# Optimization experiments

Hardware: AMD Instinct MI355X
Metric: run time of the kernel (lower is better)

Reference implementation:

```python
import jax, jax.numpy as jnp
import numpy as np

N_HEAD = 8
EPS = 1e-6  # LayerNorm2d eps


def setup_inputs() -> dict:
    key = jax.random.key(0)
    ks = jax.random.split(key, 7)
    B, C, H, W = 16, 256, 128, 128
    nh, dk, dv = N_HEAD, 32, 32
    s = 1.0 / np.sqrt(C)
    return {
        "q": jax.random.normal(ks[0], (B, C, H, W), jnp.float32),
        "k": jax.random.normal(ks[1], (B, C, H, W), jnp.float32),
        "v": jax.random.normal(ks[2], (B, C, H, W), jnp.float32),
        # 1x1 convs without bias == channel matmuls; weight shape [out_ch, in_ch]
        "wq": jax.random.normal(ks[3], (nh * dk, C), jnp.float32) * s,
        "wk": jax.random.normal(ks[4], (nh * dk, C), jnp.float32) * s,
        "wv": jax.random.normal(ks[5], (nh * dv, C), jnp.float32) * s,
        "wfc": jax.random.normal(ks[6], (C, nh * dv), jnp.float32) * (1.0 / np.sqrt(nh * dv)),
        "ln_w": jnp.ones((C,), jnp.float32),
        "ln_b": jnp.zeros((C,), jnp.float32),
        "kernel": 5,
        "pad": 2,
    }


def _forward(q, k, v, wq, wk, wv, wfc, ln_w, ln_b, kernel, pad):
    B, C, H, W = q.shape
    nh = N_HEAD
    dk = wq.shape[0] // nh
    dv = wv.shape[0] // nh
    assert kernel == 2 * pad + 1
    residual = q
    # 1x1 conv projections, split into heads: [B, nh, d, H, W]
    qh = jnp.einsum('oc,bchw->bohw', wq, q).reshape(B, nh, dk, H, W)
    kh = jnp.einsum('oc,bchw->bohw', wk, k).reshape(B, nh, dk, H, W)
    vh = jnp.einsum('oc,bchw->bohw', wv, v).reshape(B, nh, dv, H, W)
    # zero-pad spatially: out-of-bounds correlations/values are zero, matching the
    # original bilinear sampler (zeros padding) and the custom padding() helper.
    kp = jnp.pad(kh, ((0, 0), (0, 0), (0, 0), (pad, pad), (pad, pad)))
    vp = jnp.pad(vh, ((0, 0), (0, 0), (0, 0), (pad, pad), (pad, pad)))
    # local correlation volume: dot(q[i,j], k[i+dy-pad, j+dx-pad]) for the KxK window
    # (integer offsets -> bilinear sample degenerates to a gather). Never materializes
    # the full [B, HW, HW] matrix the torch code builds before sampling.
    corr = jnp.stack(
        [jnp.einsum('bncij,bncij->bnij', qh, kp[:, :, :, dy:dy + H, dx:dx + W])
         for dy in range(kernel) for dx in range(kernel)], axis=-1)  # [B,nh,H,W,K*K]
    # relu (from CorrBlock.corr), temperature = sqrt(d_k), softmax over window.
    # OOB entries are 0 (not -inf), faithfully matching the original.
    attn = jax.nn.softmax(jax.nn.relu(corr) / jnp.float32(np.sqrt(dk)), axis=-1)
    # channel attention: per-pixel weighted sum of v over the same window
    out = jnp.zeros((B, nh, dv, H, W), q.dtype)
    idx = 0
    for dy in range(kernel):
        for dx in range(kernel):
            out = out + attn[:, :, :, :, idx][:, :, None] * vp[:, :, :, dy:dy + H, dx:dx + W]
            idx += 1
    o = jnp.einsum('oc,bchw->bohw', wfc, out.reshape(B, nh * dv, H, W)) + residual
    # LayerNorm2d: normalize over channel dim per pixel
    mu = o.mean(1, keepdims=True)
    var = ((o - mu) ** 2).mean(1, keepdims=True)
    y = (o - mu) / jnp.sqrt(var + EPS)
    return ln_w[None, :, None, None] * y + ln_b[None, :, None, None]


def reference(q, k, v, wq, wk, wv, wfc, ln_w, ln_b, kernel, pad):
    return _forward(q, k, v, wq, wk, wv, wfc, ln_w, ln_b, kernel, pad)
```

## Files before the change

kernel.cpp:

```cpp
#include <hip/hip_runtime.h>
#include <hip/hip_bf16.h>

#define BATCH 16
#define CH 256
#define HH 128
#define WW 128
#define HWSZ (HH * WW)
#define NHEAD 8
#define DHEAD 32
#define LDST 40
#define PW 132
#define PPIX (132 * 132)

typedef __attribute__((ext_vector_type(8))) short bf16x8;
typedef __attribute__((ext_vector_type(4))) float f32x4;
typedef _Float16 h2v __attribute__((ext_vector_type(2)));

__device__ __forceinline__ unsigned short f2b(float f) {
    unsigned u = __builtin_bit_cast(unsigned, f);
    u += 0x7fffu + ((u >> 16) & 1u);
    return (unsigned short)(u >> 16);
}
__device__ __forceinline__ unsigned short f2h(float f) {
    _Float16 h = (_Float16)f;
    return __builtin_bit_cast(unsigned short, h);
}

#if __has_builtin(__builtin_amdgcn_fdot2)
#define DOT2(a, b, c) __builtin_amdgcn_fdot2((a), (b), (c), false)
#else
#define DOT2(a, b, c) ((c) + (float)(a).x * (float)(b).x + (float)(a).y * (float)(b).y)
#endif

__global__ __launch_bounds__(256)
void zpad_kernel(unsigned short* __restrict__ kpad, unsigned short* __restrict__ vpad)
{
    int bid = blockIdx.x;
    unsigned short* dst = ((bid & 1) ? vpad : kpad) + (size_t)(bid >> 1) * PPIX * DHEAD;
    const uint4 z = {0u, 0u, 0u, 0u};
    for (int i = threadIdx.x; i < 1040; i += 256) {
        int row, col;
        if (i < 264)      { row = i / 132; col = i - row * 132; }
        else if (i < 528) { int j = i - 264; int r = j / 132; row = 130 + r; col = j - r * 132; }
        else              { int j = i - 528; row = 2 + (j >> 2); int c = j & 3; col = (c < 2) ? c : (128 + c); }
        uint4* p = reinterpret_cast<uint4*>(dst + (size_t)(row * PW + col) * DHEAD);
        p[0] = z; p[1] = z; p[2] = z; p[3] = z;
    }
}

__global__ __launch_bounds__(256)
void prep_kernel(const float* __restrict__ wq, const float* __restrict__ wk,
                 const float* __restrict__ wv, unsigned short* __restrict__ wb)
{
    const float* src = (blockIdx.y == 0) ? wq : (blockIdx.y == 1) ? wk : wv;
    unsigned short* dst = wb + blockIdx.y * 65536;
    int e = (blockIdx.x * 256 + threadIdx.x) * 8;
    const float4* s = reinterpret_cast<const float4*>(src + e);
    float4 a = s[0], c = s[1];
    uint4 u;
    u.x = (unsigned)f2b(a.x) | ((unsigned)f2b(a.y) << 16);
    u.y = (unsigned)f2b(a.z) | ((unsigned)f2b(a.w) << 16);
    u.z = (unsigned)f2b(c.x) | ((unsigned)f2b(c.y) << 16);
    u.w = (unsigned)f2b(c.z) | ((unsigned)f2b(c.w) << 16);
    *reinterpret_cast<uint4*>(dst + e) = u;
}

__global__ __launch_bounds__(256)
void proj_kernel(const float* __restrict__ q, const float* __restrict__ k,
                 const float* __restrict__ v, const unsigned short* __restrict__ wb,
                 unsigned short* __restrict__ qh, unsigned short* __restrict__ kpad,
                 unsigned short* __restrict__ vpad)
{
    __shared__ __align__(16) unsigned short lA[256 * LDST];
    __shared__ __align__(16) unsigned short lB[64 * LDST];

    const int t = threadIdx.x;
    const int b = blockIdx.y;
    const int p0 = blockIdx.x * 64;
    const int z = blockIdx.z;

    const float* X; unsigned short* Y;
    if (z == 0)      { X = q; Y = qh; }
    else if (z == 1) { X = k; Y = kpad; }
    else             { X = v; Y = vpad; }
    const unsigned short* Wb = wb + z * 65536;
    X += (size_t)b * CH * HWSZ;
    const size_t pixstride = (z == 0) ? (size_t)HWSZ : (size_t)PPIX;
    Y += (size_t)b * NHEAD * pixstride * DHEAD;

    const int lane = t & 63;
    const int wid  = t >> 6;
    const int lrow = lane & 15;
    const int lkg  = lane >> 4;
    const int pB = t & 63;
    const int cg = t >> 6;

    f32x4 acc[4][4];
    const f32x4 zero = {0.f, 0.f, 0.f, 0.f};
#pragma unroll
    for (int m = 0; m < 4; ++m)
#pragma unroll
        for (int n = 0; n < 4; ++n) acc[m][n] = zero;

    for (int ks = 0; ks < 8; ++ks) {
        const int k0 = ks * 32;
#pragma unroll
        for (int r = 0; r < 4; ++r) {
            int idx = t + 256 * r;
            int o = idx >> 2, kc = idx & 3;
            uint4 wv4 = *reinterpret_cast<const uint4*>(Wb + o * 256 + k0 + kc * 8);
            *reinterpret_cast<uint4*>(&lA[o * LDST + kc * 8]) = wv4;
        }
        {
            const float* xp = X + (size_t)(k0 + cg * 8) * HWSZ + p0 + pB;
            float fv[8];
#pragma unroll
            for (int i = 0; i < 8; ++i) fv[i] = xp[(size_t)i * HWSZ];
            ushort4 h0, h1;
            h0.x = f2b(fv[0]); h0.y = f2b(fv[1]); h0.z = f2b(fv[2]); h0.w = f2b(fv[3]);
            h1.x = f2b(fv[4]); h1.y = f2b(fv[5]); h1.z = f2b(fv[6]); h1.w = f2b(fv[7]);
            *reinterpret_cast<ushort4*>(&lB[pB * LDST + cg * 8])     = h0;
            *reinterpret_cast<ushort4*>(&lB[pB * LDST + cg * 8 + 4]) = h1;
        }
        __syncthreads();

        bf16x8 af[4], bfv[4];
#pragma unroll
        for (int m = 0; m < 4; ++m)
            af[m] = *reinterpret_cast<const bf16x8*>(&lA[(wid * 64 + m * 16 + lrow) * LDST + lkg * 8]);
#pragma unroll
        for (int n = 0; n < 4; ++n)
            bfv[n] = *reinterpret_cast<const bf16x8*>(&lB[(n * 16 + lrow) * LDST + lkg * 8]);
#pragma unroll
        for (int m = 0; m < 4; ++m)
#pragma unroll
            for (int n = 0; n < 4; ++n)
                acc[m][n] = __builtin_amdgcn_mfma_f32_16x16x32_bf16(af[m], bfv[n], acc[m][n], 0, 0, 0);
        __syncthreads();
    }

    const int lr = lane >> 4, lc = lane & 15;
#pragma unroll
    for (int m = 0; m < 4; ++m)
#pragma unroll
        for (int n = 0; n < 4; ++n) {
            int o = wid * 64 + m * 16 + lr * 4;
            int hh_ = o >> 5, d0 = o & 31;
            int p = p0 + n * 16 + lc;
            ushort4 pk;
            pk.x = f2h(acc[m][n][0]); pk.y = f2h(acc[m][n][1]);
            pk.z = f2h(acc[m][n][2]); pk.w = f2h(acc[m][n][3]);
            size_t pix;
            if (z == 0) pix = (size_t)hh_ * HWSZ + p;
            else { int row = p >> 7, col = p & 127; pix = (size_t)hh_ * PPIX + (size_t)(row + 2) * PW + (col + 2); }
            *reinterpret_cast<ushort4*>(&Y[pix * DHEAD + d0]) = pk;
        }
}

__global__ __launch_bounds__(1024)
void attn_kernel(unsigned short* __restrict__ qh,
                 const unsigned short* __restrict__ kpad,
                 const unsigned short* __restrict__ vpad)
{
    const int t = threadIdx.x;
    const int swz = (blockIdx.x & 7) * 1024 + (blockIdx.x >> 3);
    const int bh = swz >> 6;
    const int tile = swz & 63;
    const int x0 = (tile & 7) * 16, y0 = (tile >> 3) * 16;
    const int qc = t & 3;
    const int px = (t >> 2) & 15;
    const int py = t >> 6;
    const int gx = x0 + px, gy = y0 + py;

    unsigned short* qp = qh + ((size_t)bh * HWSZ + gy * WW + gx) * DHEAD + qc * 8;
    const unsigned short* kb = kpad + (size_t)bh * PPIX * DHEAD + qc * 8;
    const unsigned short* vb = vpad + (size_t)bh * PPIX * DHEAD + qc * 8;

    union { uint4 u; h2v h2[4]; } Q;
    Q.u = *reinterpret_cast<const uint4*>(qp);

    float ew[25];
#pragma unroll
    for (int wy = 0; wy < 5; ++wy) {
        const unsigned short* krow = kb + (size_t)((gy + wy) * PW + gx) * DHEAD;
#pragma unroll
        for (int wx = 0; wx < 5; ++wx) {
            union { uint4 u; h2v h2[4]; } K;
            K.u = *reinterpret_cast<const uint4*>(krow + wx * DHEAD);
            float s = 0.f;
#pragma unroll
            for (int j = 0; j < 4; ++j)
                s = DOT2(Q.h2[j], K.h2[j], s);
            s += __shfl_xor(s, 1);
            s += __shfl_xor(s, 2);
            ew[wy * 5 + wx] = __expf(fmaxf(s, 0.f) * 0.17677669529663687f);
        }
    }

    float sum = 0.f;
#pragma unroll
    for (int i = 0; i < 25; ++i) sum += ew[i];
    const float inv = 1.f / sum;

    union { uint4 u; h2v h2[4]; } A;
    const h2v hz = {(_Float16)0.f, (_Float16)0.f};
#pragma unroll
    for (int j = 0; j < 4; ++j) A.h2[j] = hz;

#pragma unroll
    for (int wy = 0; wy < 5; ++wy) {
        const unsigned short* vrow = vb + (size_t)((gy + wy) * PW + gx) * DHEAD;
#pragma unroll
        for (int wx = 0; wx < 5; ++wx) {
            _Float16 wh = (_Float16)(ew[wy * 5 + wx] * inv);
            h2v w2 = {wh, wh};
            union { uint4 u; h2v h2[4]; } V;
            V.u = *reinterpret_cast<const uint4*>(vrow + wx * DHEAD);
#pragma unroll
            for (int j = 0; j < 4; ++j)
                A.h2[j] += w2 * V.h2[j];
        }
    }

    *reinterpret_cast<uint4*>(qp) = A.u;
}

__global__ __launch_bounds__(256)
void fcln_kernel(const unsigned short* __restrict__ ob, const float* __restrict__ wfc,
                 const float* __restrict__ qres, const float* __restrict__ lnw,
                 const float* __restrict__ lnb, float* __restrict__ out)
{
    __shared__ __align__(16) unsigned short lA[256 * LDST];
    __shared__ __align__(16) unsigned short lB[64 * LDST];
    __shared__ float lsum[4][64];
    __shared__ float lssq[4][64];

    const int t = threadIdx.x;
    const int b = blockIdx.y;
    const int p0 = blockIdx.x * 64;

    const int lane = t & 63;
    const int wid  = t >> 6;
    const int lrow = lane & 15;
    const int lkg  = lane >> 4;
    const int pxs = t >> 2, qcs = t & 3;

    f32x4 acc[4][4];
    const f32x4 zero = {0.f, 0.f, 0.f, 0.f};
#pragma unroll
    for (int m = 0; m < 4; ++m)
#pragma unroll
        for (int n = 0; n < 4; ++n) acc[m][n] = zero;

    for (int ks = 0; ks < 8; ++ks) {
        const int k0 = ks * 32;
        {
            const float4* wr = reinterpret_cast<const float4*>(wfc + t * 256 + k0);
#pragma unroll
            for (int i = 0; i < 8; ++i) {
                float4 f = wr[i];
                ushort4 hh;
                hh.x = f2b(f.x); hh.y = f2b(f.y); hh.z = f2b(f.z); hh.w = f2b(f.w);
                *reinterpret_cast<ushort4*>(&lA[t * LDST + i * 4]) = hh;
            }
        }
        {
            const unsigned short* obb = ob + (size_t)(b * NHEAD + ks) * HWSZ * DHEAD;
            uint4 bv = *reinterpret_cast<const uint4*>(obb + (size_t)(p0 + pxs) * DHEAD + qcs * 8);
            uint4 o4;
            {
                h2v h;
                h = __builtin_bit_cast(h2v, bv.x); o4.x = (unsigned)f2b((float)h.x) | ((unsigned)f2b((float)h.y) << 16);
                h = __builtin_bit_cast(h2v, bv.y); o4.y = (unsigned)f2b((float)h.x) | ((unsigned)f2b((float)h.y) << 16);
                h = __builtin_bit_cast(h2v, bv.z); o4.z = (unsigned)f2b((float)h.x) | ((unsigned)f2b((float)h.y) << 16);
                h = __builtin_bit_cast(h2v, bv.w); o4.w = (unsigned)f2b((float)h.x) | ((unsigned)f2b((float)h.y) << 16);
            }
            *reinterpret_cast<uint4*>(&lB[pxs * LDST + qcs * 8]) = o4;
        }
        __syncthreads();

        bf16x8 af[4], bfv[4];
#pragma unroll
        for (int m = 0; m < 4; ++m)
            af[m] = *reinterpret_cast<const bf16x8*>(&lA[(wid * 64 + m * 16 + lrow) * LDST + lkg * 8]);
#pragma unroll
        for (int n = 0; n < 4; ++n)
            bfv[n] = *reinterpret_cast<const bf16x8*>(&lB[(n * 16 + lrow) * LDST + lkg * 8]);
#pragma unroll
        for (int m = 0; m < 4; ++m)
#pragma unroll
            for (int n = 0; n < 4; ++n)
                acc[m][n] = __builtin_amdgcn_mfma_f32_16x16x32_bf16(af[m], bfv[n], acc[m][n], 0, 0, 0);
        __syncthreads();
    }

    const int lr = lane >> 4, lc = lane & 15;
    const float* qb = qres + (size_t)b * CH * HWSZ;
#pragma unroll
    for (int m = 0; m < 4; ++m)
#pragma unroll
        for (int n = 0; n < 4; ++n)
#pragma unroll
            for (int j = 0; j < 4; ++j) {
                int o = wid * 64 + m * 16 + lr * 4 + j;
                int p = p0 + n * 16 + lc;
                acc[m][n][j] += qb[(size_t)o * HWSZ + p];
            }

    float s[4], s2[4];
#pragma unroll
    for (int n = 0; n < 4; ++n) {
        float a = 0.f, c2 = 0.f;
#pragma unroll
        for (int m = 0; m < 4; ++m)
#pragma unroll
            for (int j = 0; j < 4; ++j) {
                float x = acc[m][n][j];
                a += x; c2 += x * x;
            }
        a  += __shfl_xor(a, 16);  a  += __shfl_xor(a, 32);
        c2 += __shfl_xor(c2, 16); c2 += __shfl_xor(c2, 32);
        s[n] = a; s2[n] = c2;
    }
    if (lane < 16) {
#pragma unroll
        for (int n = 0; n < 4; ++n) {
            lsum[wid][n * 16 + lane] = s[n];
            lssq[wid][n * 16 + lane] = s2[n];
        }
    }
    __syncthreads();

    float mu[4], rs[4];
#pragma unroll
    for (int n = 0; n < 4; ++n) {
        int p = n * 16 + lc;
        float ts = lsum[0][p] + lsum[1][p] + lsum[2][p] + lsum[3][p];
        float tq = lssq[0][p] + lssq[1][p] + lssq[2][p] + lssq[3][p];
        float m_ = ts * (1.f / 256.f);
        float v_ = tq * (1.f / 256.f) - m_ * m_;
        mu[n] = m_;
        rs[n] = rsqrtf(v_ + 1e-6f);
    }

    float* op = out + (size_t)b * CH * HWSZ;
#pragma unroll
    for (int m = 0; m < 4; ++m)
#pragma unroll
        for (int j = 0; j < 4; ++j) {
            int o = wid * 64 + m * 16 + lr * 4 + j;
            float g = lnw[o], bb = lnb[o];
#pragma unroll
            for (int n = 0; n < 4; ++n) {
                int p = p0 + n * 16 + lc;
                op[(size_t)o * HWSZ + p] = (acc[m][n][j] - mu[n]) * rs[n] * g + bb;
            }
        }
}

extern "C" void kernel_launch(void* const* d_in, const int* in_sizes, int n_in,
                              void* d_out, int out_size, void* d_ws, size_t ws_size,
                              hipStream_t stream) {
    const float* q   = (const float*)d_in[0];
    const float* k   = (const float*)d_in[1];
    const float* v   = (const float*)d_in[2];
    const float* wq  = (const float*)d_in[3];
    const float* wk  = (const float*)d_in[4];
    const float* wv  = (const float*)d_in[5];
    const float* wfc = (const float*)d_in[6];
    const float* lnw = (const float*)d_in[7];
    const float* lnb = (const float*)d_in[8];

    const size_t qsz = (size_t)BATCH * NHEAD * HWSZ * DHEAD;
    const size_t psz = (size_t)BATCH * NHEAD * PPIX * DHEAD;
    if (ws_size < (qsz + 2 * psz) * sizeof(unsigned short)) return;

    unsigned short* qh = (unsigned short*)d_ws;
    unsigned short* kp = qh + qsz;
    unsigned short* vp = kp + psz;
    unsigned short* wb = (unsigned short*)d_out;

    zpad_kernel<<<256, 256, 0, stream>>>(kp, vp);
    prep_kernel<<<dim3(32, 3), 256, 0, stream>>>(wq, wk, wv, wb);
    proj_kernel<<<dim3(HWSZ / 64, BATCH, 3), 256, 0, stream>>>(q, k, v, wb, qh, kp, vp);
    attn_kernel<<<8192, 1024, 0, stream>>>(qh, kp, vp);
    fcln_kernel<<<dim3(HWSZ / 64, BATCH), 256, 0, stream>>>(qh, wfc, q, lnw, lnb, (float*)d_out);
}
```

Before: 806.2 us.

## Read weights straight from global memory, double-buffer swizzled LDS tiles in projection GEMMs

```diff
diff --git a/kernel.cpp b/kernel.cpp
--- a/kernel.cpp
+++ b/kernel.cpp
@@ -8,7 +8,6 @@
 #define HWSZ (HH * WW)
 #define NHEAD 8
 #define DHEAD 32
-#define LDST 40
 #define PW 132
 #define PPIX (132 * 132)
 
@@ -50,9 +49,11 @@
 
 __global__ __launch_bounds__(256)
 void prep_kernel(const float* __restrict__ wq, const float* __restrict__ wk,
-                 const float* __restrict__ wv, unsigned short* __restrict__ wb)
-{
-    const float* src = (blockIdx.y == 0) ? wq : (blockIdx.y == 1) ? wk : wv;
+                 const float* __restrict__ wv, const float* __restrict__ wfc,
+                 unsigned short* __restrict__ wb)
+{
+    const float* src = (blockIdx.y == 0) ? wq : (blockIdx.y == 1) ? wk
+                     : (blockIdx.y == 2) ? wv : wfc;
     unsigned short* dst = wb + blockIdx.y * 65536;
     int e = (blockIdx.x * 256 + threadIdx.x) * 8;
     const float4* s = reinterpret_cast<const float4*>(src + e);
@@ -65,18 +66,17 @@
     *reinterpret_cast<uint4*>(dst + e) = u;
 }
 
-__global__ __launch_bounds__(256)
+__global__ __launch_bounds__(512)
 void proj_kernel(const float* __restrict__ q, const float* __restrict__ k,
                  const float* __restrict__ v, const unsigned short* __restrict__ wb,
                  unsigned short* __restrict__ qh, unsigned short* __restrict__ kpad,
                  unsigned short* __restrict__ vpad)
 {
-    __shared__ __align__(16) unsigned short lA[256 * LDST];
-    __shared__ __align__(16) unsigned short lB[64 * LDST];
+    __shared__ __align__(16) unsigned short lB[2][128 * 32];
 
     const int t = threadIdx.x;
     const int b = blockIdx.y;
-    const int p0 = blockIdx.x * 64;
+    const int p0 = blockIdx.x * 128;
     const int z = blockIdx.z;
 
     const float* X; unsigned short* Y;
@@ -90,10 +90,12 @@
 
     const int lane = t & 63;
     const int wid  = t >> 6;
+    const int wm   = wid & 3;
+    const int wn   = wid >> 2;
     const int lrow = lane & 15;
     const int lkg  = lane >> 4;
-    const int pB = t & 63;
-    const int cg = t >> 6;
+    const int pB   = t & 127;
+    const int cg   = t >> 7;
 
     f32x4 acc[4][4];
     const f32x4 zero = {0.f, 0.f, 0.f, 0.f};
@@ -104,39 +106,32 @@
 
     for (int ks = 0; ks < 8; ++ks) {
         const int k0 = ks * 32;
-#pragma unroll
-        for (int r = 0; r < 4; ++r) {
-            int idx = t + 256 * r;
-            int o = idx >> 2, kc = idx & 3;
-            uint4 wv4 = *reinterpret_cast<const uint4*>(Wb + o * 256 + k0 + kc * 8);
-            *reinterpret_cast<uint4*>(&lA[o * LDST + kc * 8]) = wv4;
-        }
         {
             const float* xp = X + (size_t)(k0 + cg * 8) * HWSZ + p0 + pB;
             float fv[8];
 #pragma unroll
             for (int i = 0; i < 8; ++i) fv[i] = xp[(size_t)i * HWSZ];
-            ushort4 h0, h1;
-            h0.x = f2b(fv[0]); h0.y = f2b(fv[1]); h0.z = f2b(fv[2]); h0.w = f2b(fv[3]);
-            h1.x = f2b(fv[4]); h1.y = f2b(fv[5]); h1.z = f2b(fv[6]); h1.w = f2b(fv[7]);
-            *reinterpret_cast<ushort4*>(&lB[pB * LDST + cg * 8])     = h0;
-            *reinterpret_cast<ushort4*>(&lB[pB * LDST + cg * 8 + 4]) = h1;
+            uint4 u;
+            u.x = (unsigned)f2b(fv[0]) | ((unsigned)f2b(fv[1]) << 16);
+            u.y = (unsigned)f2b(fv[2]) | ((unsigned)f2b(fv[3]) << 16);
+            u.z = (unsigned)f2b(fv[4]) | ((unsigned)f2b(fv[5]) << 16);
+            u.w = (unsigned)f2b(fv[6]) | ((unsigned)f2b(fv[7]) << 16);
+            *reinterpret_cast<uint4*>(&lB[ks & 1][pB * 32 + ((cg ^ (pB & 3)) << 3)]) = u;
         }
         __syncthreads();
 
         bf16x8 af[4], bfv[4];
 #pragma unroll
         for (int m = 0; m < 4; ++m)
-            af[m] = *reinterpret_cast<const bf16x8*>(&lA[(wid * 64 + m * 16 + lrow) * LDST + lkg * 8]);
+            af[m] = *reinterpret_cast<const bf16x8*>(Wb + (wm * 64 + m * 16 + lrow) * 256 + k0 + lkg * 8);
 #pragma unroll
         for (int n = 0; n < 4; ++n)
-            bfv[n] = *reinterpret_cast<const bf16x8*>(&lB[(n * 16 + lrow) * LDST + lkg * 8]);
+            bfv[n] = *reinterpret_cast<const bf16x8*>(&lB[ks & 1][(wn * 64 + n * 16 + lrow) * 32 + ((lkg ^ (lrow & 3)) << 3)]);
 #pragma unroll
         for (int m = 0; m < 4; ++m)
 #pragma unroll
             for (int n = 0; n < 4; ++n)
                 acc[m][n] = __builtin_amdgcn_mfma_f32_16x16x32_bf16(af[m], bfv[n], acc[m][n], 0, 0, 0);
-        __syncthreads();
     }
 
     const int lr = lane >> 4, lc = lane & 15;
@@ -144,9 +139,9 @@
     for (int m = 0; m < 4; ++m)
 #pragma unroll
         for (int n = 0; n < 4; ++n) {
-            int o = wid * 64 + m * 16 + lr * 4;
+            int o = wm * 64 + m * 16 + lr * 4;
             int hh_ = o >> 5, d0 = o & 31;
-            int p = p0 + n * 16 + lc;
+            int p = p0 + wn * 64 + n * 16 + lc;
             ushort4 pk;
             pk.x = f2h(acc[m][n][0]); pk.y = f2h(acc[m][n][1]);
             pk.z = f2h(acc[m][n][2]); pk.w = f2h(acc[m][n][3]);
@@ -225,25 +220,27 @@
     *reinterpret_cast<uint4*>(qp) = A.u;
 }
 
-__global__ __launch_bounds__(256)
-void fcln_kernel(const unsigned short* __restrict__ ob, const float* __restrict__ wfc,
+__global__ __launch_bounds__(512)
+void fcln_kernel(const unsigned short* __restrict__ ob, const unsigned short* __restrict__ wfcb,
                  const float* __restrict__ qres, const float* __restrict__ lnw,
                  const float* __restrict__ lnb, float* __restrict__ out)
 {
-    __shared__ __align__(16) unsigned short lA[256 * LDST];
-    __shared__ __align__(16) unsigned short lB[64 * LDST];
-    __shared__ float lsum[4][64];
-    __shared__ float lssq[4][64];
+    __shared__ __align__(16) unsigned short lB[2][128 * 32];
+    __shared__ float lsum[8][128];
+    __shared__ float lssq[8][128];
 
     const int t = threadIdx.x;
     const int b = blockIdx.y;
-    const int p0 = blockIdx.x * 64;
+    const int p0 = blockIdx.x * 128;
 
     const int lane = t & 63;
     const int wid  = t >> 6;
+    const int wm   = wid & 3;
+    const int wn   = wid >> 2;
     const int lrow = lane & 15;
     const int lkg  = lane >> 4;
-    const int pxs = t >> 2, qcs = t & 3;
+    const int pxs  = t >> 2;
+    const int qcs  = t & 3;
 
     f32x4 acc[4][4];
     const f32x4 zero = {0.f, 0.f, 0.f, 0.f};
@@ -254,16 +251,6 @@
 
     for (int ks = 0; ks < 8; ++ks) {
         const int k0 = ks * 32;
-        {
-            const float4* wr = reinterpret_cast<const float4*>(wfc + t * 256 + k0);
-#pragma unroll
-            for (int i = 0; i < 8; ++i) {
-                float4 f = wr[i];
-                ushort4 hh;
-                hh.x = f2b(f.x); hh.y = f2b(f.y); hh.z = f2b(f.z); hh.w = f2b(f.w);
-                *reinterpret_cast<ushort4*>(&lA[t * LDST + i * 4]) = hh;
-            }
-        }
         {
             const unsigned short* obb = ob + (size_t)(b * NHEAD + ks) * HWSZ * DHEAD;
             uint4 bv = *reinterpret_cast<const uint4*>(obb + (size_t)(p0 + pxs) * DHEAD + qcs * 8);
@@ -275,23 +262,22 @@
                 h = __builtin_bit_cast(h2v, bv.z); o4.z = (unsigned)f2b((float)h.x) | ((unsigned)f2b((float)h.y) << 16);
                 h = __builtin_bit_cast(h2v, bv.w); o4.w = (unsigned)f2b((float)h.x) | ((unsigned)f2b((float)h.y) << 16);
             }
-            *reinterpret_cast<uint4*>(&lB[pxs * LDST + qcs * 8]) = o4;
+            *reinterpret_cast<uint4*>(&lB[ks & 1][pxs * 32 + ((qcs ^ (pxs & 3)) << 3)]) = o4;
         }
         __syncthreads();
 
         bf16x8 af[4], bfv[4];
 #pragma unroll
         for (int m = 0; m < 4; ++m)
-            af[m] = *reinterpret_cast<const bf16x8*>(&lA[(wid * 64 + m * 16 + lrow) * LDST + lkg * 8]);
+            af[m] = *reinterpret_cast<const bf16x8*>(wfcb + (wm * 64 + m * 16 + lrow) * 256 + k0 + lkg * 8);
 #pragma unroll
         for (int n = 0; n < 4; ++n)
-            bfv[n] = *reinterpret_cast<const bf16x8*>(&lB[(n * 16 + lrow) * LDST + lkg * 8]);
+            bfv[n] = *reinterpret_cast<const bf16x8*>(&lB[ks & 1][(wn * 64 + n * 16 + lrow) * 32 + ((lkg ^ (lrow & 3)) << 3)]);
 #pragma unroll
         for (int m = 0; m < 4; ++m)
 #pragma unroll
             for (int n = 0; n < 4; ++n)
                 acc[m][n] = __builtin_amdgcn_mfma_f32_16x16x32_bf16(af[m], bfv[n], acc[m][n], 0, 0, 0);
-        __syncthreads();
     }
 
     const int lr = lane >> 4, lc = lane & 15;
@@ -302,8 +288,8 @@
         for (int n = 0; n < 4; ++n)
 #pragma unroll
             for (int j = 0; j < 4; ++j) {
-                int o = wid * 64 + m * 16 + lr * 4 + j;
-                int p = p0 + n * 16 + lc;
+                int o = wm * 64 + m * 16 + lr * 4 + j;
+                int p = p0 + wn * 64 + n * 16 + lc;
                 acc[m][n][j] += qb[(size_t)o * HWSZ + p];
             }
 
@@ -322,11 +308,12 @@
         c2 += __shfl_xor(c2, 16); c2 += __shfl_xor(c2, 32);
         s[n] = a; s2[n] = c2;
     }
+    __syncthreads();
     if (lane < 16) {
 #pragma unroll
         for (int n = 0; n < 4; ++n) {
-            lsum[wid][n * 16 + lane] = s[n];
-            lssq[wid][n * 16 + lane] = s2[n];
+            lsum[wid][wn * 64 + n * 16 + lane] = s[n];
+            lssq[wid][wn * 64 + n * 16 + lane] = s2[n];
         }
     }
     __syncthreads();
@@ -334,9 +321,9 @@
     float mu[4], rs[4];
 #pragma unroll
     for (int n = 0; n < 4; ++n) {
-        int p = n * 16 + lc;
-        float ts = lsum[0][p] + lsum[1][p] + lsum[2][p] + lsum[3][p];
-        float tq = lssq[0][p] + lssq[1][p] + lssq[2][p] + lssq[3][p];
+        int p = wn * 64 + n * 16 + lc;
+        float ts = lsum[wn * 4 + 0][p] + lsum[wn * 4 + 1][p] + lsum[wn * 4 + 2][p] + lsum[wn * 4 + 3][p];
+        float tq = lssq[wn * 4 + 0][p] + lssq[wn * 4 + 1][p] + lssq[wn * 4 + 2][p] + lssq[wn * 4 + 3][p];
         float m_ = ts * (1.f / 256.f);
         float v_ = tq * (1.f / 256.f) - m_ * m_;
         mu[n] = m_;
@@ -348,11 +335,11 @@
     for (int m = 0; m < 4; ++m)
 #pragma unroll
         for (int j = 0; j < 4; ++j) {
-            int o = wid * 64 + m * 16 + lr * 4 + j;
+            int o = wm * 64 + m * 16 + lr * 4 + j;
             float g = lnw[o], bb = lnb[o];
 #pragma unroll
             for (int n = 0; n < 4; ++n) {
-                int p = p0 + n * 16 + lc;
+                int p = p0 + wn * 64 + n * 16 + lc;
                 op[(size_t)o * HWSZ + p] = (acc[m][n][j] - mu[n]) * rs[n] * g + bb;
             }
         }
@@ -373,16 +360,16 @@
 
     const size_t qsz = (size_t)BATCH * NHEAD * HWSZ * DHEAD;
     const size_t psz = (size_t)BATCH * NHEAD * PPIX * DHEAD;
-    if (ws_size < (qsz + 2 * psz) * sizeof(unsigned short)) return;
+    if (ws_size < (qsz + 2 * psz + 4 * 65536) * sizeof(unsigned short)) return;
 
     unsigned short* qh = (unsigned short*)d_ws;
     unsigned short* kp = qh + qsz;
     unsigned short* vp = kp + psz;
-    unsigned short* wb = (unsigned short*)d_out;
+    unsigned short* wb = vp + psz;
 
     zpad_kernel<<<256, 256, 0, stream>>>(kp, vp);
-    prep_kernel<<<dim3(32, 3), 256, 0, stream>>>(wq, wk, wv, wb);
-    proj_kernel<<<dim3(HWSZ / 64, BATCH, 3), 256, 0, stream>>>(q, k, v, wb, qh, kp, vp);
+    prep_kernel<<<dim3(32, 4), 256, 0, stream>>>(wq, wk, wv, wfc, wb);
+    proj_kernel<<<dim3(HWSZ / 128, BATCH, 3), 512, 0, stream>>>(q, k, v, wb, qh, kp, vp);
     attn_kernel<<<8192, 1024, 0, stream>>>(qh, kp, vp);
-    fcln_kernel<<<dim3(HWSZ / 64, BATCH), 256, 0, stream>>>(qh, wfc, q, lnw, lnb, (float*)d_out);
-}
+    fcln_kernel<<<dim3(HWSZ / 128, BATCH), 512, 0, stream>>>(qh, wb + 3 * 65536, q, lnw, lnb, (float*)d_out);
+}
```

New measurement: 868.6 us. 1.08x slower.

## Double-buffer GEMM operands, load weights from global into registers, prebake bf16 wfc

Applied to the files above, without the earlier changes.

```diff
diff --git a/kernel.cpp b/kernel.cpp
--- a/kernel.cpp
+++ b/kernel.cpp
@@ -8,9 +8,9 @@
 #define HWSZ (HH * WW)
 #define NHEAD 8
 #define DHEAD 32
-#define LDST 40
 #define PW 132
 #define PPIX (132 * 132)
+#define LDSTB 40
 
 typedef __attribute__((ext_vector_type(8))) short bf16x8;
 typedef __attribute__((ext_vector_type(4))) float f32x4;
@@ -25,11 +25,15 @@
     _Float16 h = (_Float16)f;
     return __builtin_bit_cast(unsigned short, h);
 }
+__device__ __forceinline__ unsigned pkbf(float a, float b) {
+    __hip_bfloat162_raw r = __hip_bfloat162_raw(__float22bfloat162_rn(make_float2(a, b)));
+    return (unsigned)r.x | ((unsigned)r.y << 16);
+}
 
 #if __has_builtin(__builtin_amdgcn_fdot2)
 #define DOT2(a, b, c) __builtin_amdgcn_fdot2((a), (b), (c), false)
 #else
-#define DOT2(a, b, c) ((c) + (float)(a).x * (float)(b).x + (float)(a).y * (float)(b).y)
+#define DOT2(a, b, c) ((c) + (float)(a)[0] * (float)(b)[0] + (float)(a)[1] * (float)(b)[1])
 #endif
 
 __global__ __launch_bounds__(256)
@@ -50,18 +54,18 @@
 
 __global__ __launch_bounds__(256)
 void prep_kernel(const float* __restrict__ wq, const float* __restrict__ wk,
-                 const float* __restrict__ wv, unsigned short* __restrict__ wb)
-{
-    const float* src = (blockIdx.y == 0) ? wq : (blockIdx.y == 1) ? wk : wv;
+                 const float* __restrict__ wv, const float* __restrict__ wfc,
+                 unsigned short* __restrict__ wb)
+{
+    const float* src = (blockIdx.y == 0) ? wq : (blockIdx.y == 1) ? wk
+                     : (blockIdx.y == 2) ? wv : wfc;
     unsigned short* dst = wb + blockIdx.y * 65536;
     int e = (blockIdx.x * 256 + threadIdx.x) * 8;
     const float4* s = reinterpret_cast<const float4*>(src + e);
     float4 a = s[0], c = s[1];
     uint4 u;
-    u.x = (unsigned)f2b(a.x) | ((unsigned)f2b(a.y) << 16);
-    u.y = (unsigned)f2b(a.z) | ((unsigned)f2b(a.w) << 16);
-    u.z = (unsigned)f2b(c.x) | ((unsigned)f2b(c.y) << 16);
-    u.w = (unsigned)f2b(c.z) | ((unsigned)f2b(c.w) << 16);
+    u.x = pkbf(a.x, a.y); u.y = pkbf(a.z, a.w);
+    u.z = pkbf(c.x, c.y); u.w = pkbf(c.z, c.w);
     *reinterpret_cast<uint4*>(dst + e) = u;
 }
 
@@ -71,8 +75,7 @@
                  unsigned short* __restrict__ qh, unsigned short* __restrict__ kpad,
                  unsigned short* __restrict__ vpad)
 {
-    __shared__ __align__(16) unsigned short lA[256 * LDST];
-    __shared__ __align__(16) unsigned short lB[64 * LDST];
+    __shared__ __align__(16) unsigned short lB[2][64 * LDSTB];
 
     const int t = threadIdx.x;
     const int b = blockIdx.y;
@@ -92,8 +95,19 @@
     const int wid  = t >> 6;
     const int lrow = lane & 15;
     const int lkg  = lane >> 4;
-    const int pB = t & 63;
-    const int cg = t >> 6;
+    const int pB   = t & 63;
+    const int cg   = t >> 6;
+
+    float fv[8];
+    {
+        const float* xp = X + (size_t)(cg * 8) * HWSZ + p0 + pB;
+#pragma unroll
+        for (int i = 0; i < 8; ++i) fv[i] = xp[(size_t)i * HWSZ];
+    }
+    bf16x8 afc[4], afn[4];
+#pragma unroll
+    for (int m = 0; m < 4; ++m)
+        afc[m] = *reinterpret_cast<const bf16x8*>(Wb + (wid * 64 + m * 16 + lrow) * 256 + lkg * 8);
 
     f32x4 acc[4][4];
     const f32x4 zero = {0.f, 0.f, 0.f, 0.f};
@@ -103,40 +117,34 @@
         for (int n = 0; n < 4; ++n) acc[m][n] = zero;
 
     for (int ks = 0; ks < 8; ++ks) {
-        const int k0 = ks * 32;
-#pragma unroll
-        for (int r = 0; r < 4; ++r) {
-            int idx = t + 256 * r;
-            int o = idx >> 2, kc = idx & 3;
-            uint4 wv4 = *reinterpret_cast<const uint4*>(Wb + o * 256 + k0 + kc * 8);
-            *reinterpret_cast<uint4*>(&lA[o * LDST + kc * 8]) = wv4;
-        }
         {
-            const float* xp = X + (size_t)(k0 + cg * 8) * HWSZ + p0 + pB;
-            float fv[8];
+            uint4 u;
+            u.x = pkbf(fv[0], fv[1]); u.y = pkbf(fv[2], fv[3]);
+            u.z = pkbf(fv[4], fv[5]); u.w = pkbf(fv[6], fv[7]);
+            *reinterpret_cast<uint4*>(&lB[ks & 1][pB * LDSTB + cg * 8]) = u;
+        }
+        if (ks < 7) {
+            const float* xp = X + (size_t)((ks + 1) * 32 + cg * 8) * HWSZ + p0 + pB;
 #pragma unroll
             for (int i = 0; i < 8; ++i) fv[i] = xp[(size_t)i * HWSZ];
-            ushort4 h0, h1;
-            h0.x = f2b(fv[0]); h0.y = f2b(fv[1]); h0.z = f2b(fv[2]); h0.w = f2b(fv[3]);
-            h1.x = f2b(fv[4]); h1.y = f2b(fv[5]); h1.z = f2b(fv[6]); h1.w = f2b(fv[7]);
-            *reinterpret_cast<ushort4*>(&lB[pB * LDST + cg * 8])     = h0;
-            *reinterpret_cast<ushort4*>(&lB[pB * LDST + cg * 8 + 4]) = h1;
         }
         __syncthreads();
-
-        bf16x8 af[4], bfv[4];
+        if (ks < 7) {
+#pragma unroll
+            for (int m = 0; m < 4; ++m)
+                afn[m] = *reinterpret_cast<const bf16x8*>(Wb + (wid * 64 + m * 16 + lrow) * 256 + (ks + 1) * 32 + lkg * 8);
+        }
+        bf16x8 bfv[4];
+#pragma unroll
+        for (int n = 0; n < 4; ++n)
+            bfv[n] = *reinterpret_cast<const bf16x8*>(&lB[ks & 1][(n * 16 + lrow) * LDSTB + lkg * 8]);
 #pragma unroll
         for (int m = 0; m < 4; ++m)
-            af[m] = *reinterpret_cast<const bf16x8*>(&lA[(wid * 64 + m * 16 + lrow) * LDST + lkg * 8]);
-#pragma unroll
-        for (int n = 0; n < 4; ++n)
-            bfv[n] = *reinterpret_cast<const bf16x8*>(&lB[(n * 16 + lrow) * LDST + lkg * 8]);
-#pragma unroll
-        for (int m = 0; m < 4; ++m)
 #pragma unroll
             for (int n = 0; n < 4; ++n)
-                acc[m][n] = __builtin_amdgcn_mfma_f32_16x16x32_bf16(af[m], bfv[n], acc[m][n], 0, 0, 0);
-        __syncthreads();
+                acc[m][n] = __builtin_amdgcn_mfma_f32_16x16x32_bf16(afc[m], bfv[n], acc[m][n], 0, 0, 0);
+#pragma unroll
+        for (int m = 0; m < 4; ++m) afc[m] = afn[m];
     }
 
     const int lr = lane >> 4, lc = lane & 15;
@@ -222,16 +230,20 @@
         }
     }
 
-    *reinterpret_cast<uint4*>(qp) = A.u;
+    uint4 o;
+    o.x = pkbf((float)A.h2[0][0], (float)A.h2[0][1]);
+    o.y = pkbf((float)A.h2[1][0], (float)A.h2[1][1]);
+    o.z = pkbf((float)A.h2[2][0], (float)A.h2[2][1]);
+    o.w = pkbf((float)A.h2[3][0], (float)A.h2[3][1]);
+    *reinterpret_cast<uint4*>(qp) = o;
 }
 
 __global__ __launch_bounds__(256)
-void fcln_kernel(const unsigned short* __restrict__ ob, const float* __restrict__ wfc,
+void fcln_kernel(const unsigned short* __restrict__ ob, const unsigned short* __restrict__ wfcb,
                  const float* __restrict__ qres, const float* __restrict__ lnw,
                  const float* __restrict__ lnb, float* __restrict__ out)
 {
-    __shared__ __align__(16) unsigned short lA[256 * LDST];
-    __shared__ __align__(16) unsigned short lB[64 * LDST];
+    __shared__ __align__(16) unsigned short lB[2][64 * LDSTB];
     __shared__ float lsum[4][64];
     __shared__ float lssq[4][64];
 
@@ -243,7 +255,18 @@
     const int wid  = t >> 6;
     const int lrow = lane & 15;
     const int lkg  = lane >> 4;
-    const int pxs = t >> 2, qcs = t & 3;
+    const int pxs  = t >> 2;
+    const int qcs  = t & 3;
+
+    uint4 bv;
+    {
+        const unsigned short* obb = ob + (size_t)(b * NHEAD + 0) * HWSZ * DHEAD;
+        bv = *reinterpret_cast<const uint4*>(obb + (size_t)(p0 + pxs) * DHEAD + qcs * 8);
+    }
+    bf16x8 afc[4], afn[4];
+#pragma unroll
+    for (int m = 0; m < 4; ++m)
+        afc[m] = *reinterpret_cast<const bf16x8*>(wfcb + (wid * 64 + m * 16 + lrow) * 256 + lkg * 8);
 
     f32x4 acc[4][4];
     const f32x4 zero = {0.f, 0.f, 0.f, 0.f};
@@ -253,45 +276,28 @@
         for (int n = 0; n < 4; ++n) acc[m][n] = zero;
 
     for (int ks = 0; ks < 8; ++ks) {
-        const int k0 = ks * 32;
-        {
-            const float4* wr = reinterpret_cast<const float4*>(wfc + t * 256 + k0);
-#pragma unroll
-            for (int i = 0; i < 8; ++i) {
-                float4 f = wr[i];
-                ushort4 hh;
-                hh.x = f2b(f.x); hh.y = f2b(f.y); hh.z = f2b(f.z); hh.w = f2b(f.w);
-                *reinterpret_cast<ushort4*>(&lA[t * LDST + i * 4]) = hh;
-            }
-        }
-        {
-            const unsigned short* obb = ob + (size_t)(b * NHEAD + ks) * HWSZ * DHEAD;
-            uint4 bv = *reinterpret_cast<const uint4*>(obb + (size_t)(p0 + pxs) * DHEAD + qcs * 8);
-            uint4 o4;
-            {
-                h2v h;
-                h = __builtin_bit_cast(h2v, bv.x); o4.x = (unsigned)f2b((float)h.x) | ((unsigned)f2b((float)h.y) << 16);
-                h = __builtin_bit_cast(h2v, bv.y); o4.y = (unsigned)f2b((float)h.x) | ((unsigned)f2b((float)h.y) << 16);
-                h = __builtin_bit_cast(h2v, bv.z); o4.z = (unsigned)f2b((float)h.x) | ((unsigned)f2b((float)h.y) << 16);
-                h = __builtin_bit_cast(h2v, bv.w); o4.w = (unsigned)f2b((float)h.x) | ((unsigned)f2b((float)h.y) << 16);
-            }
-            *reinterpret_cast<uint4*>(&lB[pxs * LDST + qcs * 8]) = o4;
+        *reinterpret_cast<uint4*>(&lB[ks & 1][pxs * LDSTB + qcs * 8]) = bv;
+        if (ks < 7) {
+            const unsigned short* obb = ob + (size_t)(b * NHEAD + ks + 1) * HWSZ * DHEAD;
+            bv = *reinterpret_cast<const uint4*>(obb + (size_t)(p0 + pxs) * DHEAD + qcs * 8);
         }
         __syncthreads();
-
-        bf16x8 af[4], bfv[4];
+        if (ks < 7) {
+#pragma unroll
+            for (int m = 0; m < 4; ++m)
+                afn[m] = *reinterpret_cast<const bf16x8*>(wfcb + (wid * 64 + m * 16 + lrow) * 256 + (ks + 1) * 32 + lkg * 8);
+        }
+        bf16x8 bfv[4];
+#pragma unroll
+        for (int n = 0; n < 4; ++n)
+            bfv[n] = *reinterpret_cast<const bf16x8*>(&lB[ks & 1][(n * 16 + lrow) * LDSTB + lkg * 8]);
 #pragma unroll
         for (int m = 0; m < 4; ++m)
-            af[m] = *reinterpret_cast<const bf16x8*>(&lA[(wid * 64 + m * 16 + lrow) * LDST + lkg * 8]);
-#pragma unroll
-        for (int n = 0; n < 4; ++n)
-            bfv[n] = *reinterpret_cast<const bf16x8*>(&lB[(n * 16 + lrow) * LDST + lkg * 8]);
-#pragma unroll
-        for (int m = 0; m < 4; ++m)
 #pragma unroll
             for (int n = 0; n < 4; ++n)
-                acc[m][n] = __builtin_amdgcn_mfma_f32_16x16x32_bf16(af[m], bfv[n], acc[m][n], 0, 0, 0);
-        __syncthreads();
+                acc[m][n] = __builtin_amdgcn_mfma_f32_16x16x32_bf16(afc[m], bfv[n], acc[m][n], 0, 0, 0);
+#pragma unroll
+        for (int m = 0; m < 4; ++m) afc[m] = afn[m];
     }
 
     const int lr = lane >> 4, lc = lane & 15;
@@ -373,16 +379,16 @@
 
     const size_t qsz = (size_t)BATCH * NHEAD * HWSZ * DHEAD;
     const size_t psz = (size_t)BATCH * NHEAD * PPIX * DHEAD;
-    if (ws_size < (qsz + 2 * psz) * sizeof(unsigned short)) return;
+    if (ws_size < (qsz + 2 * psz + 4 * 65536) * sizeof(unsigned short)) return;
 
     unsigned short* qh = (unsigned short*)d_ws;
     unsigned short* kp = qh + qsz;
     unsigned short* vp = kp + psz;
-    unsigned short* wb = (unsigned short*)d_out;
+    unsigned short* wb = vp + psz;
 
     zpad_kernel<<<256, 256, 0, stream>>>(kp, vp);
-    prep_kernel<<<dim3(32, 3), 256, 0, stream>>>(wq, wk, wv, wb);
+    prep_kernel<<<dim3(32, 4), 256, 0, stream>>>(wq, wk, wv, wfc, wb);
     proj_kernel<<<dim3(HWSZ / 64, BATCH, 3), 256, 0, stream>>>(q, k, v, wb, qh, kp, vp);
     attn_kernel<<<8192, 1024, 0, stream>>>(qh, kp, vp);
-    fcln_kernel<<<dim3(HWSZ / 64, BATCH), 256, 0, stream>>>(qh, wfc, q, lnw, lnb, (float*)d_out);
-}
+    fcln_kernel<<<dim3(HWSZ / 64, BATCH), 256, 0, stream>>>(qh, wb + 3 * 65536, q, lnw, lnb, (float*)d_out);
+}
```

Measured after the change: 798.5 us. About the same (-1.0%).
